# Kernel tuning notes

Measured on AMD Instinct MI355X. Metric: run time of the kernel, lower is better.

## Reference

```python
import jax, jax.numpy as jnp
import numpy as np

EMB = 768
HEADS = 12
DK = EMB // HEADS


def setup_inputs() -> dict:
    key = jax.random.key(0)
    ks = jax.random.split(key, 11)
    B, S = 2, 2048
    lim = 1.0 / np.sqrt(EMB)
    def lin(k):
        kw, kb = jax.random.split(k)
        W = jax.random.uniform(kw, (EMB, EMB), jnp.float32, -lim, lim)
        b = jax.random.uniform(kb, (EMB,), jnp.float32, -lim, lim)
        return W, b
    Wq, bq = lin(ks[0])
    Wk, bk = lin(ks[1])
    Wv, bv = lin(ks[2])
    Wo, bo = lin(ks[3])
    return {
        "query": jax.random.normal(ks[4], (B, S, EMB), jnp.float32),
        "key": jax.random.normal(ks[5], (B, S, EMB), jnp.float32),
        "value": jax.random.normal(ks[6], (B, S, EMB), jnp.float32),
        "Wq": Wq, "bq": bq, "Wk": Wk, "bk": bk,
        "Wv": Wv, "bv": bv, "Wo": Wo, "bo": bo,
    }


def reference(query, key, value, Wq, bq, Wk, bk, Wv, bv, Wo, bo):
    B, S, _ = query.shape
    # nn.Linear: x @ W^T + b, then split heads -> [B, H, S, d_k]
    def proj(x, W, b):
        return (x @ W.T + b).reshape(B, -1, HEADS, DK).transpose(0, 2, 1, 3)
    q = proj(query, Wq, bq)
    k = proj(key, Wk, bk)
    v = proj(value, Wv, bv)
    scale = 1.0 / jnp.sqrt(jnp.float32(DK))
    scores = jnp.einsum('bhqd,bhkd->bhqk', q, k) * scale  # [B,H,S,S]
    attn = jax.nn.softmax(scores, axis=-1)
    av = jnp.einsum('bhqk,bhkd->bhqd', attn, v)
    concat = av.transpose(0, 2, 1, 3).reshape(B, -1, EMB)
    return concat @ Wo.T + bo
```

## Files before the change

### kernel.cpp

```cpp
#include <hip/hip_runtime.h>
#include <hip/hip_bf16.h>

#define EMB 768
#define HEADS 12
#define DKV 64
#define BATCH 2
#define SEQ 2048
#define NTOK (BATCH*SEQ)

typedef float f32x4 __attribute__((ext_vector_type(4)));
typedef unsigned short u16;
typedef u16 u16x8 __attribute__((ext_vector_type(8)));
typedef u16 u16x4 __attribute__((ext_vector_type(4)));
typedef __bf16 bf16x8 __attribute__((ext_vector_type(8)));

__device__ __forceinline__ u16 f2bf(float f) {
  return __builtin_bit_cast(u16, (__bf16)f);
}
__device__ __forceinline__ float fexp2(float x) {
#if __has_builtin(__builtin_amdgcn_exp2f)
  return __builtin_amdgcn_exp2f(x);
#else
  return exp2f(x);
#endif
}
__device__ __forceinline__ f32x4 mfma16(u16x8 a, u16x8 b, f32x4 c) {
  return __builtin_amdgcn_mfma_f32_16x16x32_bf16(
      __builtin_bit_cast(bf16x8, a), __builtin_bit_cast(bf16x8, b), c, 0, 0, 0);
}
__device__ __forceinline__ void gload16(const void* g, void* l) {
  __builtin_amdgcn_global_load_lds(
      (const __attribute__((address_space(1))) void*)g,
      (__attribute__((address_space(3))) void*)l, 16, 0, 0);
}

__global__ void cast_w_k(
    const float* __restrict__ w0, const float* __restrict__ w1,
    const float* __restrict__ w2, const float* __restrict__ w3,
    u16* __restrict__ W0, u16* __restrict__ W1, u16* __restrict__ W2, u16* __restrict__ W3)
{
  const int NW = EMB*EMB/8;
  int i = blockIdx.x*256 + threadIdx.x;
  if (i >= 4*NW) return;
  int which = i / NW, off = i - which*NW;
  const float* s = which==0 ? w0 : which==1 ? w1 : which==2 ? w2 : w3;
  u16* d        = which==0 ? W0 : which==1 ? W1 : which==2 ? W2 : W3;
  float4 a = reinterpret_cast<const float4*>(s)[off*2];
  float4 b = reinterpret_cast<const float4*>(s)[off*2+1];
  u16x8 o;
  o[0]=f2bf(a.x); o[1]=f2bf(a.y); o[2]=f2bf(a.z); o[3]=f2bf(a.w);
  o[4]=f2bf(b.x); o[5]=f2bf(b.y); o[6]=f2bf(b.z); o[7]=f2bf(b.w);
  reinterpret_cast<u16x8*>(d)[off] = o;
}

template<int MODE, bool AF32>
__device__ __forceinline__ void gemm_core(
    const void* __restrict__ Ap, const u16* __restrict__ Bm,
    const float* __restrict__ bias, float ascale, float bscale,
    void* __restrict__ outp, u16* __restrict__ At, u16* __restrict__ Bt,
    int m0, int n0)
{
  const int t = threadIdx.x;
  const int w = t >> 6, lane = t & 63, lg = lane >> 4, lr = lane & 15;
  const int wr = w >> 1, wc = w & 1;
  const int lrow = lane >> 3, csl = lane & 7;

  f32x4 acc[2][4] = {};
  f32x4 raf[2][2];

  auto A_LOAD = [&](int kb) {
    #pragma unroll
    for (int q2 = 0; q2 < 2; ++q2) {
      int c = q2*256 + t, row = c >> 3, sl = c & 7;
      const float* p = (const float*)Ap + (size_t)(m0+row)*EMB + kb + sl*8;
      raf[q2][0] = *reinterpret_cast<const f32x4*>(p);
      raf[q2][1] = *reinterpret_cast<const f32x4*>(p + 4);
    }
  };
  auto A_WRITE = [&](int bi) {
    #pragma unroll
    for (int q2 = 0; q2 < 2; ++q2) {
      int c = q2*256 + t, row = c >> 3, sl = c & 7;
      u16x8 v;
      #pragma unroll
      for (int j = 0; j < 4; ++j) {
        v[j]   = f2bf(raf[q2][0][j] * ascale);
        v[4+j] = f2bf(raf[q2][1][j] * ascale);
      }
      *reinterpret_cast<u16x8*>(&At[bi*4096 + row*64 + ((sl ^ (row & 7))*8)]) = v;
    }
  };
  auto A_GLOAD = [&](int kb, int bi) {
    #pragma unroll
    for (int i = 0; i < 2; ++i) {
      int ci = w*2 + i;
      int row = ci*8 + lrow;
      int sg = csl ^ (row & 7);
      gload16((const u16*)Ap + (size_t)(m0+row)*EMB + kb + sg*8,
              &At[bi*4096 + ci*512]);
    }
  };
  auto B_GLOAD = [&](int kb, int bi) {
    #pragma unroll
    for (int i = 0; i < 4; ++i) {
      int ci = w*4 + i;
      int row = ci*8 + lrow;
      int sg = csl ^ (row & 7);
      gload16(Bm + (size_t)(n0+row)*EMB + kb + sg*8, &Bt[bi*8192 + ci*512]);
    }
  };

  auto COMPUTE = [&](int bi) {
    u16x8 af[2][2], bf[4][2];
    #pragma unroll
    for (int fm = 0; fm < 2; ++fm)
      #pragma unroll
      for (int kk = 0; kk < 2; ++kk) {
        int r = wr*32 + fm*16 + lr;
        int p = (lg + 4*kk) ^ (r & 7);
        af[fm][kk] = *reinterpret_cast<const u16x8*>(&At[bi*4096 + r*64 + p*8]);
      }
    #pragma unroll
    for (int fn = 0; fn < 4; ++fn)
      #pragma unroll
      for (int kk = 0; kk < 2; ++kk) {
        int r = wc*64 + fn*16 + lr;
        int p = (lg + 4*kk) ^ (r & 7);
        bf[fn][kk] = *reinterpret_cast<const u16x8*>(&Bt[bi*8192 + r*64 + p*8]);
      }
    __builtin_amdgcn_s_setprio(1);
    #pragma unroll
    for (int fm = 0; fm < 2; ++fm)
      #pragma unroll
      for (int fn = 0; fn < 4; ++fn)
        #pragma unroll
        for (int kk = 0; kk < 2; ++kk)
          acc[fm][fn] = mfma16(af[fm][kk], bf[fn][kk], acc[fm][fn]);
    __builtin_amdgcn_s_setprio(0);
  };

  const int NSTEP = EMB/64;
  if constexpr (AF32) {
    A_LOAD(0);
    B_GLOAD(0, 0);
    A_WRITE(0);
    __syncthreads();
    #pragma unroll
    for (int ts = 0; ts < NSTEP; ++ts) {
      if (ts+1 < NSTEP) {
        A_LOAD((ts+1)*64);
        B_GLOAD((ts+1)*64, (ts & 1) ^ 1);
      }
      COMPUTE(ts & 1);
      if (ts+1 < NSTEP) {
        A_WRITE((ts & 1) ^ 1);
        __syncthreads();
      }
    }
  } else {
    A_GLOAD(0, 0);
    B_GLOAD(0, 0);
    __syncthreads();
    #pragma unroll
    for (int ts = 0; ts < NSTEP; ++ts) {
      if (ts+1 < NSTEP) {
        A_GLOAD((ts+1)*64, (ts & 1) ^ 1);
        B_GLOAD((ts+1)*64, (ts & 1) ^ 1);
      }
      COMPUTE(ts & 1);
      if (ts+1 < NSTEP) __syncthreads();
    }
  }

  #pragma unroll
  for (int fm = 0; fm < 2; ++fm)
    #pragma unroll
    for (int fn = 0; fn < 4; ++fn) {
      const int mb = m0 + wr*32 + fm*16 + lg*4;
      const int e  = n0 + wc*64 + fn*16 + lr;
      if constexpr (MODE == 2) {
        int bb = mb >> 11, sb = mb & 2047, h = e >> 6, d = e & 63;
        u16x4 o4;
        #pragma unroll
        for (int j = 0; j < 4; ++j) o4[j] = f2bf(acc[fm][fn][j] + bias[e]*bscale);
        *reinterpret_cast<u16x4*>(
            reinterpret_cast<u16*>(outp) + (((size_t)(bb*HEADS+h))*DKV + d)*SEQ + sb) = o4;
      } else {
        #pragma unroll
        for (int j = 0; j < 4; ++j) {
          int m = mb + j;
          float val = acc[fm][fn][j] + bias[e]*bscale;
          if constexpr (MODE == 0) {
            int bb = m >> 11, s = m & 2047, h = e >> 6, d = e & 63;
            reinterpret_cast<u16*>(outp)[(((size_t)(bb*HEADS+h))*SEQ + s)*DKV + d] = f2bf(val);
          } else {
            reinterpret_cast<float*>(outp)[(size_t)m*EMB + e] = val;
          }
        }
      }
    }
}

__global__ __launch_bounds__(256) void qkv_k(
    const float* __restrict__ Xq, const float* __restrict__ Xk, const float* __restrict__ Xv,
    const u16* __restrict__ Wq, const u16* __restrict__ Wk, const u16* __restrict__ Wv,
    const float* __restrict__ bq, const float* __restrict__ bk, const float* __restrict__ bv,
    u16* __restrict__ Qh, u16* __restrict__ Kh, u16* __restrict__ Vh, float csc)
{
  __shared__ __align__(16) u16 At[2*64*64];
  __shared__ __align__(16) u16 Bt[2*128*64];
  const int m0 = blockIdx.x*64, n0 = blockIdx.y*128;
  const int z = blockIdx.z;
  if (z == 0)
    gemm_core<0,true>(Xq, Wq, bq, csc, csc, Qh, At, Bt, m0, n0);
  else if (z == 1)
    gemm_core<0,true>(Xk, Wk, bk, 1.f, 1.f, Kh, At, Bt, m0, n0);
  else
    gemm_core<2,true>(Xv, Wv, bv, 1.f, 1.f, Vh, At, Bt, m0, n0);
}

__global__ __launch_bounds__(256) void gemm_out_k(
    const u16* __restrict__ A, const u16* __restrict__ Bm,
    const float* __restrict__ bias, float* __restrict__ outp)
{
  __shared__ __align__(16) u16 At[2*64*64];
  __shared__ __align__(16) u16 Bt[2*128*64];
  gemm_core<1,false>(A, Bm, bias, 1.f, 1.f, outp, At, Bt, blockIdx.x*64, blockIdx.y*128);
}

__global__ __launch_bounds__(256) void flash_attn_k(
    const u16* __restrict__ Q, const u16* __restrict__ K, const u16* __restrict__ VT,
    u16* __restrict__ av)
{
  __shared__ __align__(16) u16 Kt[2][64*64];
  __shared__ __align__(16) u16 Vt[2][64*64];
  __shared__ __align__(16) u16 Pt[4][16*64];

  const int t = threadIdx.x;
  const int w = t >> 6, lane = t & 63, lg = lane >> 4, lr = lane & 15;
  const int qb = blockIdx.x;
  const int bh = blockIdx.y;
  const u16* Qb = Q  + (size_t)bh*SEQ*DKV;
  const u16* Kb = K  + (size_t)bh*SEQ*DKV;
  const u16* Vb = VT + (size_t)bh*DKV*SEQ;

  const int qrow = qb*64 + w*16 + lr;
  u16x8 qf[2];
  qf[0] = *reinterpret_cast<const u16x8*>(Qb + (size_t)qrow*DKV + lg*8);
  qf[1] = *reinterpret_cast<const u16x8*>(Qb + (size_t)qrow*DKV + 32 + lg*8);

  f32x4 acc[4] = {};
  float mrun = -1e30f, lrun = 0.f;

  auto STAGE = [&](int kt0, int bi) {
    #pragma unroll
    for (int c2 = 0; c2 < 2; ++c2) {
      int c = c2*256 + t;
      int row = c >> 3, sl = c & 7;
      int sg = sl ^ (row & 7);
      gload16(Kb + (size_t)(kt0+row)*DKV + sg*8, &Kt[bi][c*8]);
    }
    #pragma unroll
    for (int c2 = 0; c2 < 2; ++c2) {
      int c = c2*256 + t;
      int row = c >> 3, sl = c & 7;
      int sg = sl ^ (row & 7);
      gload16(Vb + (size_t)row*SEQ + kt0 + sg*8, &Vt[bi][c*8]);
    }
  };

  const int NT = SEQ/64;
  char* Pw = reinterpret_cast<char*>(&Pt[w][0]);

#define TILE(bi, kt)                                                          \
  do {                                                                        \
    if ((kt)+1 < NT) STAGE(((kt)+1)*64, (bi)^1);    \
    f32x4 s[4];                                                               \
    __builtin_amdgcn_s_setprio(1);                                            \
    _Pragma("unroll")                                                         \
    for (int fc = 0; fc < 4; ++fc) {                                          \
      f32x4 z = {};                                                           \
      _Pragma("unroll")                                                       \
      for (int kk = 0; kk < 2; ++kk) {                                        \
        int r = fc*16 + lr;                                                   \
        int slot = (lg + 4*kk) ^ (r & 7);                                     \
        u16x8 kf = *reinterpret_cast<const u16x8*>(&Kt[bi][r*64 + slot*8]);   \
        z = mfma16(kf, qf[kk], z);                                            \
      }                                                                       \
      s[fc] = z;                                                              \
    }                                                                         \
    __builtin_amdgcn_s_setprio(0);                                            \
    float a0 = fmaxf(fmaxf(s[0][0], s[0][1]), s[0][2]);                       \
    float a1 = fmaxf(fmaxf(s[0][3], s[1][0]), s[1][1]);                       \
    float a2 = fmaxf(fmaxf(s[1][2], s[1][3]), s[2][0]);                       \
    float a3 = fmaxf(fmaxf(s[2][1], s[2][2]), s[2][3]);                       \
    float a4 = fmaxf(fmaxf(s[3][0], s[3][1]), s[3][2]);                       \
    float pmax = fmaxf(fmaxf(fmaxf(a0, a1), a2),                              \
                       fmaxf(fmaxf(a3, a4), s[3][3]));                        \
    if (__any(pmax > mrun + 8.f)) {          \
      float pm = fmaxf(pmax, __shfl_xor(pmax, 16));                           \
      pm = fmaxf(pm, __shfl_xor(pm, 32));                                     \
      float mnew = fmaxf(mrun, pm);                                           \
      float corr = fexp2(mrun - mnew);                                        \
      mrun = mnew; lrun *= corr;                                              \
      _Pragma("unroll")                                                       \
      for (int fc = 0; fc < 4; ++fc)                                          \
        _Pragma("unroll")                                                     \
        for (int j = 0; j < 4; ++j)                                           \
          acc[fc][j] *= corr;                                                 \
    }                                                                         \
    float p[4][4], rs[4];                                                     \
    _Pragma("unroll")                                                         \
    for (int fc = 0; fc < 4; ++fc) {                                          \
      _Pragma("unroll")                                                       \
      for (int j = 0; j < 4; ++j) p[fc][j] = fexp2(s[fc][j] - mrun);          \
      rs[fc] = (p[fc][0] + p[fc][1]) + (p[fc][2] + p[fc][3]);                 \
    }                                                                         \
    lrun += (rs[0] + rs[1]) + (rs[2] + rs[3]);      \
    _Pragma("unroll")                                                         \
    for (int fc = 0; fc < 4; ++fc) {                                          \
      u16x4 q4;                                                               \
      _Pragma("unroll")                                                       \
      for (int j = 0; j < 4; ++j) q4[j] = f2bf(p[fc][j]);                     \
      *reinterpret_cast<u16x4*>(                                              \
          Pw + lr*128 + (((fc*4 + lg) ^ ((lr & 7) << 1))*8)) = q4;            \
    }                                                                         \
    asm volatile("s_waitcnt lgkmcnt(0)" ::: "memory");                        \
    __builtin_amdgcn_sched_barrier(0);                                        \
    __builtin_amdgcn_s_setprio(1);                                            \
    _Pragma("unroll")                                                         \
    for (int kk = 0; kk < 2; ++kk) {                                          \
      u16x8 pf = *reinterpret_cast<const u16x8*>(                             \
          Pw + lr*128 + (((kk*8 + lg*2) ^ ((lr & 7) << 1))*8));               \
      _Pragma("unroll")                                                       \
      for (int fc = 0; fc < 4; ++fc) {                                        \
        int rv = fc*16 + lr;                                                  \
        int slotv = (lg + 4*kk) ^ (rv & 7);                                   \
        u16x8 vf = *reinterpret_cast<const u16x8*>(&Vt[bi][rv*64 + slotv*8]); \
        acc[fc] = mfma16(vf, pf, acc[fc]);                                    \
      }                                                                       \
    }                                                                         \
    __builtin_amdgcn_s_setprio(0);                                            \
    __syncthreads();   \
  } while (0)

  STAGE(0, 0);
  __syncthreads();
  for (int kt = 0; kt < NT; kt += 2) {
    TILE(0, kt);
    TILE(1, kt+1);
  }
#undef TILE

  float lt = lrun;
  lt += __shfl_xor(lt, 16);
  lt += __shfl_xor(lt, 32);
  const float inv = 1.0f / lt;

  const int b = bh / HEADS, h = bh % HEADS;
  #pragma unroll
  for (int fc = 0; fc < 4; ++fc) {
    u16x4 o4;
    #pragma unroll
    for (int j = 0; j < 4; ++j) o4[j] = f2bf(acc[fc][j] * inv);
    *reinterpret_cast<u16x4*>(
        av + ((size_t)(b*SEQ + qrow))*EMB + h*64 + fc*16 + lg*4) = o4;
  }
}

extern "C" void kernel_launch(void* const* d_in, const int* in_sizes, int n_in,
                              void* d_out, int out_size, void* d_ws, size_t ws_size,
                              hipStream_t stream) {
  const float* xq_f = (const float*)d_in[0];
  const float* xk_f = (const float*)d_in[1];
  const float* xv_f = (const float*)d_in[2];
  const float* Wq = (const float*)d_in[3];
  const float* bq = (const float*)d_in[4];
  const float* Wk = (const float*)d_in[5];
  const float* bk = (const float*)d_in[6];
  const float* Wv = (const float*)d_in[7];
  const float* bv = (const float*)d_in[8];
  const float* Wo = (const float*)d_in[9];
  const float* bo = (const float*)d_in[10];

  const size_t NX = (size_t)NTOK*EMB;
  const size_t NW = (size_t)EMB*EMB;
  u16* Wc0 = (u16*)d_ws;
  u16* Wc1 = Wc0 + NW;
  u16* Wc2 = Wc1 + NW;
  u16* Wc3 = Wc2 + NW;
  u16* Qh  = Wc3 + NW;
  u16* Kh  = Qh + NX;
  u16* Vh  = Kh + NX;
  u16* Xb  = Vh + NX;

  const float csc = 0.125f * 1.4426950408889634f;

  cast_w_k<<<dim3(4*EMB*EMB/8/256), dim3(256), 0, stream>>>(
      Wq, Wk, Wv, Wo, Wc0, Wc1, Wc2, Wc3);

  qkv_k<<<dim3(NTOK/64, EMB/128, 3), dim3(256), 0, stream>>>(
      xq_f, xk_f, xv_f, Wc0, Wc1, Wc2, bq, bk, bv, Qh, Kh, Vh, csc);

  flash_attn_k<<<dim3(SEQ/64, BATCH*HEADS), dim3(256), 0, stream>>>(Qh, Kh, Vh, Xb);

  gemm_out_k<<<dim3(NTOK/64, EMB/128), dim3(256), 0, stream>>>(Xb, Wc3, bo, (float*)d_out);
}
```

Measured before the change: 95.66 us.

## Process two query sub-tiles per wave in flash attention, halving block threads

Each wave now handles 32 query rows (two 16-row fragments) instead of 16, and the block shrinks to 128 threads (2 waves) while the 64-row query tile per block stays the same. Each K/V fragment read from LDS now feeds two MFMAs, halving LDS read traffic per FLOP and giving more independent MFMA chains. The cost is roughly double the accumulator and score registers per thread, fewer waves per block for latency hiding, and more load instructions per thread when staging.

```diff
diff --git a/kernel.cpp b/kernel.cpp
--- a/kernel.cpp
+++ b/kernel.cpp
@@ -228,13 +228,13 @@
   gemm_core<1,false>(A, Bm, bias, 1.f, 1.f, outp, At, Bt, blockIdx.x*64, blockIdx.y*128);
 }
 
-__global__ __launch_bounds__(256) void flash_attn_k(
+__global__ __launch_bounds__(128) void flash_attn_k(
     const u16* __restrict__ Q, const u16* __restrict__ K, const u16* __restrict__ VT,
     u16* __restrict__ av)
 {
   __shared__ __align__(16) u16 Kt[2][64*64];
   __shared__ __align__(16) u16 Vt[2][64*64];
-  __shared__ __align__(16) u16 Pt[4][16*64];
+  __shared__ __align__(16) u16 Pt[2][2][16*64];
 
   const int t = threadIdx.x;
   const int w = t >> 6, lane = t & 63, lg = lane >> 4, lr = lane & 15;
@@ -244,25 +244,28 @@
   const u16* Kb = K  + (size_t)bh*SEQ*DKV;
   const u16* Vb = VT + (size_t)bh*DKV*SEQ;
 
-  const int qrow = qb*64 + w*16 + lr;
-  u16x8 qf[2];
-  qf[0] = *reinterpret_cast<const u16x8*>(Qb + (size_t)qrow*DKV + lg*8);
-  qf[1] = *reinterpret_cast<const u16x8*>(Qb + (size_t)qrow*DKV + 32 + lg*8);
-
-  f32x4 acc[4] = {};
-  float mrun = -1e30f, lrun = 0.f;
+  const int qr0 = qb*64 + w*32 + lr;
+  u16x8 qf0[2], qf1[2];
+  qf0[0] = *reinterpret_cast<const u16x8*>(Qb + (size_t)qr0*DKV + lg*8);
+  qf0[1] = *reinterpret_cast<const u16x8*>(Qb + (size_t)qr0*DKV + 32 + lg*8);
+  qf1[0] = *reinterpret_cast<const u16x8*>(Qb + (size_t)(qr0+16)*DKV + lg*8);
+  qf1[1] = *reinterpret_cast<const u16x8*>(Qb + (size_t)(qr0+16)*DKV + 32 + lg*8);
+
+  f32x4 acc0[4] = {}, acc1[4] = {};
+  float mrun0 = -1e30f, lrun0 = 0.f;
+  float mrun1 = -1e30f, lrun1 = 0.f;
 
   auto STAGE = [&](int kt0, int bi) {
     #pragma unroll
-    for (int c2 = 0; c2 < 2; ++c2) {
-      int c = c2*256 + t;
+    for (int c4 = 0; c4 < 4; ++c4) {
+      int c = c4*128 + t;
       int row = c >> 3, sl = c & 7;
       int sg = sl ^ (row & 7);
       gload16(Kb + (size_t)(kt0+row)*DKV + sg*8, &Kt[bi][c*8]);
     }
     #pragma unroll
-    for (int c2 = 0; c2 < 2; ++c2) {
-      int c = c2*256 + t;
+    for (int c4 = 0; c4 < 4; ++c4) {
+      int c = c4*128 + t;
       int row = c >> 3, sl = c & 7;
       int sg = sl ^ (row & 7);
       gload16(Vb + (size_t)row*SEQ + kt0 + sg*8, &Vt[bi][c*8]);
@@ -270,78 +273,88 @@
   };
 
   const int NT = SEQ/64;
-  char* Pw = reinterpret_cast<char*>(&Pt[w][0]);
+  char* Pw0 = reinterpret_cast<char*>(&Pt[w][0][0]);
+  char* Pw1 = reinterpret_cast<char*>(&Pt[w][1][0]);
+
+#define SOFTPW(S, MR, LR, ACC, PB)                                            \
+  do {                                                                        \
+    float a0 = fmaxf(fmaxf(S[0][0], S[0][1]), S[0][2]);                       \
+    float a1 = fmaxf(fmaxf(S[0][3], S[1][0]), S[1][1]);                       \
+    float a2 = fmaxf(fmaxf(S[1][2], S[1][3]), S[2][0]);                       \
+    float a3 = fmaxf(fmaxf(S[2][1], S[2][2]), S[2][3]);                       \
+    float a4 = fmaxf(fmaxf(S[3][0], S[3][1]), S[3][2]);                       \
+    float pmax = fmaxf(fmaxf(fmaxf(a0, a1), a2),                              \
+                       fmaxf(fmaxf(a3, a4), S[3][3]));                        \
+    if (__any(pmax > MR + 8.f)) {                                             \
+      float pm = fmaxf(pmax, __shfl_xor(pmax, 16));                           \
+      pm = fmaxf(pm, __shfl_xor(pm, 32));                                     \
+      float mnew = fmaxf(MR, pm);                                             \
+      float corr = fexp2(MR - mnew);                                          \
+      MR = mnew; LR *= corr;                                                  \
+      _Pragma("unroll")                                                       \
+      for (int fc = 0; fc < 4; ++fc)                                          \
+        _Pragma("unroll")                                                     \
+        for (int j = 0; j < 4; ++j)                                           \
+          ACC[fc][j] *= corr;                                                 \
+    }                                                                         \
+    float p_[4][4], rs_[4];                                                   \
+    _Pragma("unroll")                                                         \
+    for (int fc = 0; fc < 4; ++fc) {                                          \
+      _Pragma("unroll")                                                       \
+      for (int j = 0; j < 4; ++j) p_[fc][j] = fexp2(S[fc][j] - MR);           \
+      rs_[fc] = (p_[fc][0] + p_[fc][1]) + (p_[fc][2] + p_[fc][3]);            \
+    }                                                                         \
+    LR += (rs_[0] + rs_[1]) + (rs_[2] + rs_[3]);                              \
+    _Pragma("unroll")                                                         \
+    for (int fc = 0; fc < 4; ++fc) {                                          \
+      u16x4 q4;                                                               \
+      _Pragma("unroll")                                                       \
+      for (int j = 0; j < 4; ++j) q4[j] = f2bf(p_[fc][j]);                    \
+      *reinterpret_cast<u16x4*>(                                              \
+          PB + lr*128 + (((fc*4 + lg) ^ ((lr & 7) << 1))*8)) = q4;            \
+    }                                                                         \
+  } while (0)
 
 #define TILE(bi, kt)                                                          \
   do {                                                                        \
-    if ((kt)+1 < NT) STAGE(((kt)+1)*64, (bi)^1);    \
-    f32x4 s[4];                                                               \
+    if ((kt)+1 < NT) STAGE(((kt)+1)*64, (bi)^1);                              \
+    f32x4 s0[4], s1[4];                                                       \
     __builtin_amdgcn_s_setprio(1);                                            \
     _Pragma("unroll")                                                         \
     for (int fc = 0; fc < 4; ++fc) {                                          \
-      f32x4 z = {};                                                           \
+      f32x4 z0 = {}, z1 = {};                                                 \
       _Pragma("unroll")                                                       \
       for (int kk = 0; kk < 2; ++kk) {                                        \
         int r = fc*16 + lr;                                                   \
         int slot = (lg + 4*kk) ^ (r & 7);                                     \
         u16x8 kf = *reinterpret_cast<const u16x8*>(&Kt[bi][r*64 + slot*8]);   \
-        z = mfma16(kf, qf[kk], z);                                            \
+        z0 = mfma16(kf, qf0[kk], z0);                                         \
+        z1 = mfma16(kf, qf1[kk], z1);                                         \
       }                                                                       \
-      s[fc] = z;                                                              \
+      s0[fc] = z0; s1[fc] = z1;                                               \
     }                                                                         \
     __builtin_amdgcn_s_setprio(0);                                            \
-    float a0 = fmaxf(fmaxf(s[0][0], s[0][1]), s[0][2]);                       \
-    float a1 = fmaxf(fmaxf(s[0][3], s[1][0]), s[1][1]);                       \
-    float a2 = fmaxf(fmaxf(s[1][2], s[1][3]), s[2][0]);                       \
-    float a3 = fmaxf(fmaxf(s[2][1], s[2][2]), s[2][3]);                       \
-    float a4 = fmaxf(fmaxf(s[3][0], s[3][1]), s[3][2]);                       \
-    float pmax = fmaxf(fmaxf(fmaxf(a0, a1), a2),                              \
-                       fmaxf(fmaxf(a3, a4), s[3][3]));                        \
-    if (__any(pmax > mrun + 8.f)) {          \
-      float pm = fmaxf(pmax, __shfl_xor(pmax, 16));                           \
-      pm = fmaxf(pm, __shfl_xor(pm, 32));                                     \
-      float mnew = fmaxf(mrun, pm);                                           \
-      float corr = fexp2(mrun - mnew);                                        \
-      mrun = mnew; lrun *= corr;                                              \
-      _Pragma("unroll")                                                       \
-      for (int fc = 0; fc < 4; ++fc)                                          \
-        _Pragma("unroll")                                                     \
-        for (int j = 0; j < 4; ++j)                                           \
-          acc[fc][j] *= corr;                                                 \
-    }                                                                         \
-    float p[4][4], rs[4];                                                     \
-    _Pragma("unroll")                                                         \
-    for (int fc = 0; fc < 4; ++fc) {                                          \
-      _Pragma("unroll")                                                       \
-      for (int j = 0; j < 4; ++j) p[fc][j] = fexp2(s[fc][j] - mrun);          \
-      rs[fc] = (p[fc][0] + p[fc][1]) + (p[fc][2] + p[fc][3]);                 \
-    }                                                                         \
-    lrun += (rs[0] + rs[1]) + (rs[2] + rs[3]);      \
-    _Pragma("unroll")                                                         \
-    for (int fc = 0; fc < 4; ++fc) {                                          \
-      u16x4 q4;                                                               \
-      _Pragma("unroll")                                                       \
-      for (int j = 0; j < 4; ++j) q4[j] = f2bf(p[fc][j]);                     \
-      *reinterpret_cast<u16x4*>(                                              \
-          Pw + lr*128 + (((fc*4 + lg) ^ ((lr & 7) << 1))*8)) = q4;            \
-    }                                                                         \
+    SOFTPW(s0, mrun0, lrun0, acc0, Pw0);                                      \
+    SOFTPW(s1, mrun1, lrun1, acc1, Pw1);                                      \
     asm volatile("s_waitcnt lgkmcnt(0)" ::: "memory");                        \
     __builtin_amdgcn_sched_barrier(0);                                        \
     __builtin_amdgcn_s_setprio(1);                                            \
     _Pragma("unroll")                                                         \
     for (int kk = 0; kk < 2; ++kk) {                                          \
-      u16x8 pf = *reinterpret_cast<const u16x8*>(                             \
-          Pw + lr*128 + (((kk*8 + lg*2) ^ ((lr & 7) << 1))*8));               \
+      int poff = (((kk*8 + lg*2) ^ ((lr & 7) << 1))*8) + lr*128;              \
+      u16x8 pf0 = *reinterpret_cast<const u16x8*>(Pw0 + poff);                \
+      u16x8 pf1 = *reinterpret_cast<const u16x8*>(Pw1 + poff);                \
       _Pragma("unroll")                                                       \
       for (int fc = 0; fc < 4; ++fc) {                                        \
         int rv = fc*16 + lr;                                                  \
         int slotv = (lg + 4*kk) ^ (rv & 7);                                   \
         u16x8 vf = *reinterpret_cast<const u16x8*>(&Vt[bi][rv*64 + slotv*8]); \
-        acc[fc] = mfma16(vf, pf, acc[fc]);                                    \
+        acc0[fc] = mfma16(vf, pf0, acc0[fc]);                                 \
+        acc1[fc] = mfma16(vf, pf1, acc1[fc]);                                 \
       }                                                                       \
     }                                                                         \
     __builtin_amdgcn_s_setprio(0);                                            \
-    __syncthreads();   \
+    __syncthreads();                                                          \
   } while (0)
 
   STAGE(0, 0);
@@ -351,20 +364,36 @@
     TILE(1, kt+1);
   }
 #undef TILE
-
-  float lt = lrun;
-  lt += __shfl_xor(lt, 16);
-  lt += __shfl_xor(lt, 32);
-  const float inv = 1.0f / lt;
+#undef SOFTPW
 
   const int b = bh / HEADS, h = bh % HEADS;
-  #pragma unroll
-  for (int fc = 0; fc < 4; ++fc) {
-    u16x4 o4;
-    #pragma unroll
-    for (int j = 0; j < 4; ++j) o4[j] = f2bf(acc[fc][j] * inv);
-    *reinterpret_cast<u16x4*>(
-        av + ((size_t)(b*SEQ + qrow))*EMB + h*64 + fc*16 + lg*4) = o4;
+  {
+    float lt = lrun0;
+    lt += __shfl_xor(lt, 16);
+    lt += __shfl_xor(lt, 32);
+    const float inv = 1.0f / lt;
+    #pragma unroll
+    for (int fc = 0; fc < 4; ++fc) {
+      u16x4 o4;
+      #pragma unroll
+      for (int j = 0; j < 4; ++j) o4[j] = f2bf(acc0[fc][j] * inv);
+      *reinterpret_cast<u16x4*>(
+          av + ((size_t)(b*SEQ + qr0))*EMB + h*64 + fc*16 + lg*4) = o4;
+    }
+  }
+  {
+    float lt = lrun1;
+    lt += __shfl_xor(lt, 16);
+    lt += __shfl_xor(lt, 32);
+    const float inv = 1.0f / lt;
+    #pragma unroll
+    for (int fc = 0; fc < 4; ++fc) {
+      u16x4 o4;
+      #pragma unroll
+      for (int j = 0; j < 4; ++j) o4[j] = f2bf(acc1[fc][j] * inv);
+      *reinterpret_cast<u16x4*>(
+          av + ((size_t)(b*SEQ + qr0 + 16))*EMB + h*64 + fc*16 + lg*4) = o4;
+    }
   }
 }
 
@@ -402,7 +431,7 @@
   qkv_k<<<dim3(NTOK/64, EMB/128, 3), dim3(256), 0, stream>>>(
       xq_f, xk_f, xv_f, Wc0, Wc1, Wc2, bq, bk, bv, Qh, Kh, Vh, csc);
 
-  flash_attn_k<<<dim3(SEQ/64, BATCH*HEADS), dim3(256), 0, stream>>>(Qh, Kh, Vh, Xb);
+  flash_attn_k<<<dim3(SEQ/64, BATCH*HEADS), dim3(128), 0, stream>>>(Qh, Kh, Vh, Xb);
 
   gemm_out_k<<<dim3(NTOK/64, EMB/128), dim3(256), 0, stream>>>(Xb, Wc3, bo, (float*)d_out);
 }
```

New measurement: 106.0 us. +10.8%, slower.
